# Optimization experiments

Measured on AMD Instinct MI355X. Metric: run time of the kernel, lower is better.

The kernel has to match this reference:

```python
import jax, jax.numpy as jnp
import numpy as np

# dims: B batch, N regions, F feature, L max seq len, A att size, E embed, D decode, V vocab
B, N, F, L, A, E, D, V = 256, 36, 2048, 26, 512, 1024, 1024, 10000
T = L - 1  # max decode steps
ARNET_W = 0.005


def _lstm(x, h, c, wih, whh, b):
    # torch.nn.LSTMCell math (b = b_ih + b_hh fused)
    g = x @ wih.T + h @ whh.T + b
    i, f, gg, o = jnp.split(g, 4, axis=1)
    c2 = jax.nn.sigmoid(f) * c + jax.nn.sigmoid(i) * jnp.tanh(gg)
    return jax.nn.sigmoid(o) * jnp.tanh(c2), c2


def setup_inputs():
    key = jax.random.key(0)
    ks = jax.random.split(key, 21)
    p = lambda k, s: jax.random.normal(k, s, jnp.float32) * 0.02
    feats = jax.random.normal(ks[0], (B, N, F), jnp.float32)
    sequences = jax.random.randint(ks[1], (B, L), 0, V)
    sizes = jax.random.randint(ks[2], (B, 1), 2, L + 1).at[0, 0].set(L)  # pin max length
    return dict(
        feats=feats, sequences=sequences, sizes=sizes,
        emb=p(ks[3], (V, E)),
        td_wih=p(ks[4], (4 * D, E + F + D)), td_whh=p(ks[5], (4 * D, D)), td_b=p(ks[6], (4 * D,)),
        lang_wih=p(ks[7], (4 * D, F + D)), lang_whh=p(ks[8], (4 * D, D)), lang_b=p(ks[9], (4 * D,)),
        attf_w=p(ks[10], (A, F)), attf_b=p(ks[11], (A,)),
        attd_w=p(ks[12], (A, D)), attd_b=p(ks[13], (A,)),
        att_w=p(ks[14], (A,)), att_b=p(ks[15], (1,)),
        out_w=p(ks[16], (V, D)), out_b=jnp.zeros((V,), jnp.float32),
        ar_wih=p(ks[17], (4 * D, D)), ar_whh=p(ks[18], (4 * D, D)), ar_b=p(ks[19], (4 * D,)),
        arl_w=p(ks[20], (D, D)), arl_b=jnp.zeros((D,), jnp.float32),
    )


def reference(feats, sequences, sizes, emb, td_wih, td_whh, td_b,
              lang_wih, lang_whh, lang_b, attf_w, attf_b, attd_w, attd_b,
              att_w, att_b, out_w, out_b, ar_wih, ar_whh, ar_b, arl_w, arl_b):
    # sort by length descending so the active set at each step is a batch prefix
    order = jnp.argsort(-sizes[:, 0])
    dec_len = sizes[order, 0] - 1          # [B]
    seq = sequences[order]                 # [B,L]
    fs = feats[order]                      # [B,N,F]
    favg = jnp.mean(fs, axis=1)            # [B,F]
    embs = emb[seq]                        # [B,L,E]
    # feature projection of the attention module is step-invariant -> hoist
    img_att = jnp.einsum('bnf,af->bna', fs, attf_w) + attf_b  # [B,N,A]

    dt = feats.dtype
    z = jnp.zeros((B, D), dt)
    carry0 = (z, z, z, z, z, z, z, jnp.zeros((), dt))

    def step(carry, xs):
        h1, c1, h2, c2, arh, arc, prev_h1, loss = carry
        e_t, t = xs
        act = t < dec_len                  # [B] rows still decoding
        am = act[:, None]
        bsz = jnp.sum(act.astype(dt))
        # top-down attention LSTM
        h1n, c1n = _lstm(jnp.concatenate([h2, favg, e_t], axis=1), h1, c1, td_wih, td_whh, td_b)
        # additive (Bahdanau) attention; dropout is identity in eval mode
        q = h1n @ attd_w.T + attd_b        # [B,A]
        scores = jnp.einsum('bna,a->bn', jax.nn.relu(q[:, None, :] + img_att), att_w) + att_b[0]
        alpha = jax.nn.softmax(scores, axis=1)
        aw = jnp.einsum('bn,bnf->bf', alpha, fs)
        # language LSTM
        h2n, c2n = _lstm(jnp.concatenate([aw, h1n], axis=1), h2, c2, lang_wih, lang_whh, lang_b)
        # arnet auxiliary LSTM reconstructing previous hidden1
        arhn, arcn = _lstm(h1n, arh, arc, ar_wih, ar_whh, ar_b)
        diff = arhn @ arl_w.T + arl_b - prev_h1
        step_loss = jnp.where(
            t > 0,
            jnp.sum(jnp.where(act, jnp.sum(diff * diff, axis=1), 0.0)) / jnp.maximum(bsz, 1.0) * ARNET_W,
            0.0)
        pred_t = jnp.where(am, h2n @ out_w.T + out_b, 0.0)  # inactive rows stay zero
        upd = lambda new, old: jnp.where(am, new, old)      # freeze state of finished rows
        carry = (upd(h1n, h1), upd(c1n, c1), upd(h2n, h2), upd(c2n, c2),
                 upd(arhn, arh), upd(arcn, arc), upd(h1n, prev_h1), loss + step_loss)
        return carry, pred_t

    xs = (jnp.swapaxes(embs[:, :T], 0, 1), jnp.arange(T))
    carry, preds = jax.lax.scan(step, carry0, xs)
    return jnp.swapaxes(preds, 0, 1), carry[-1]  # preds [B,T,V], loss_ar scalar
```

## Files before the change

### kernel.cpp

```cpp
#include <hip/hip_runtime.h>
#include <hip/hip_bf16.h>
#include <cstdio>

typedef __hip_bfloat16 bf16;
using s8v   = __attribute__((ext_vector_type(8))) short;
using f32x4 = __attribute__((ext_vector_type(4))) float;

#define BB    256
#define NIMG  36
#define FDIM  2048
#define LSEQ  26
#define TSTEP 25
#define ADIM  512
#define EDIM  1024
#define DDIM  1024
#define VDIM  10000
#define G4    4096
#define N3    4608
#define K1    5120
#define K2    4096
#define K3    2048
#define SPLT  8

__device__ inline float bf2f(bf16 x){ return __bfloat162float(x); }
__device__ inline bf16  f2bf(float x){ return __float2bfloat16(x); }
__device__ inline float sig_(float x){ return 1.0f/(1.0f + __expf(-x)); }
__device__ inline float tanh_(float x){ return tanhf(x); }

__device__ __forceinline__ void gl_lds16(const void* g, void* l){
  __builtin_amdgcn_global_load_lds(
      (__attribute__((address_space(1))) void*)g,
      (__attribute__((address_space(3))) void*)l, 16, 0, 0);
}

template<int BM, int BN>
__global__ __launch_bounds__(256, 2) void gemm_bt(
    const bf16* __restrict__ A, int lda,
    const bf16* __restrict__ Bw, int ldb,
    float* __restrict__ C, long ldc,
    int M, int Nreal, int Ktot, int nsplit,
    const float* __restrict__ bias,
    const int* __restrict__ rowmap,
    const int* __restrict__ mask,
    const int* __restrict__ nact, int t)
{
  constexpr int BK = 32;
  constexpr int AHALF = BM*BK;
  constexpr int HALF  = (BM+BN)*BK;
  __shared__ bf16 lds[2*HALF];

  const int bn = blockIdx.x, bm = blockIdx.y, bz = blockIdx.z;
  if (nact && (long)bm*BM >= (long)nact[t]) return;

  const int tid  = threadIdx.x;
  const int lane = tid & 63;
  const int wave = tid >> 6;
  const int wr = wave & 1, wc = wave >> 1;
  constexpr int TM = BM/32, TN = BN/32;

  const int ks   = Ktot / nsplit;
  const int kbeg = bz * ks;
  const long arow0 = (long)bm*BM;
  const long bcol0 = (long)bn*BN;

  constexpr int AIT = (BM*4)/256;
  constexpr int BIT = (BN*4)/256;
  const bf16* agp[AIT]; int alo[AIT];
  const bf16* bgp[BIT]; int blo[BIT];
#pragma unroll
  for (int u=0;u<AIT;u++){
    int c = tid + u*256; int r = c>>2, sl = c&3;
    int q = sl ^ ((r>>1)&3);
    long sr = arow0 + r;
    if (rowmap) sr = rowmap[sr];
    agp[u] = A + sr*(long)lda + kbeg + q*8;
    alo[u] = c*8;
  }
#pragma unroll
  for (int u=0;u<BIT;u++){
    int c = tid + u*256; int r = c>>2, sl = c&3;
    int q = sl ^ ((r>>1)&3);
    long gc = bcol0 + r;
    bgp[u] = Bw + ((gc < (long)Nreal) ? gc : 0)*(long)ldb + kbeg + q*8;
    blo[u] = AHALF + c*8;
  }

  f32x4 acc[TM][TN];
#pragma unroll
  for (int i=0;i<TM;i++)
#pragma unroll
    for (int j=0;j<TN;j++) acc[i][j] = (f32x4){0.f,0.f,0.f,0.f};

  const int m0 = lane & 15;
  const int co = (((lane>>4) ^ ((m0>>1)&3)) * 8);
  int aoff[TM], boff[TN];
#pragma unroll
  for (int i=0;i<TM;i++) aoff[i] = (wr*(BM/2) + i*16 + m0)*BK + co;
#pragma unroll
  for (int j=0;j<TN;j++) boff[j] = AHALF + (wc*(BN/2) + j*16 + m0)*BK + co;

#pragma unroll
  for (int u=0;u<AIT;u++) gl_lds16(agp[u], lds + alo[u]);
#pragma unroll
  for (int u=0;u<BIT;u++) gl_lds16(bgp[u], lds + blo[u]);
  __syncthreads();

  auto phase = [&](int bc, int bp, int kc){
    const int kp = kc + BK;
    if (kp < ks) {
      bf16* Pb = lds + bp*HALF;
#pragma unroll
      for (int u=0;u<AIT;u++) gl_lds16(agp[u] + kp, Pb + alo[u]);
#pragma unroll
      for (int u=0;u<BIT;u++) gl_lds16(bgp[u] + kp, Pb + blo[u]);
    }
    const bf16* Lb = lds + bc*HALF;
    s8v afr[TM], bfr[TN];
#pragma unroll
    for (int i=0;i<TM;i++) afr[i] = *(const s8v*)(Lb + aoff[i]);
#pragma unroll
    for (int j=0;j<TN;j++) bfr[j] = *(const s8v*)(Lb + boff[j]);
#pragma unroll
    for (int i=0;i<TM;i++)
#pragma unroll
      for (int j=0;j<TN;j++)
        acc[i][j] = __builtin_amdgcn_mfma_f32_16x16x32_bf16(afr[i], bfr[j], acc[i][j], 0, 0, 0);
    __syncthreads();
  };
  for (int kc = 0; kc < ks; kc += 2*BK) {
    phase(0, 1, kc);
    phase(1, 0, kc + BK);
  }

  float* Cz = C + (long)bz * (long)M * ldc;
  const int rq = lane >> 4;
#pragma unroll
  for (int i=0;i<TM;i++){
    long row = arow0 + wr*(BM/2) + i*16 + rq*4;
#pragma unroll
    for (int j=0;j<TN;j++){
      long col = bcol0 + wc*(BN/2) + j*16 + m0;
      if (col < (long)Nreal) {
        float bv = (bias != nullptr && bz == 0) ? bias[col] : 0.f;
#pragma unroll
        for (int r=0;r<4;r++){
          float v = acc[i][j][r] + bv;
          if (mask) v = (t < mask[row + r]) ? v : 0.f;
          Cz[(row + r)*ldc + col] = v;
        }
      }
    }
  }
}

__global__ __launch_bounds__(256) void sort_kernel(
    const int* __restrict__ sizesp, int* __restrict__ order,
    int* __restrict__ dec, float* __restrict__ bszf, int* __restrict__ nact,
    int* __restrict__ rowmap)
{
  __shared__ int ssz[BB], so[BB], sd[BB];
  int b = threadIdx.x;
  ssz[b] = sizesp[b];
  __syncthreads();
  int s = ssz[b];
  int rank = 0;
  for (int j=0;j<BB;j++){
    int sj = ssz[j];
    rank += (sj > s) || (sj == s && j < b);
  }
  so[rank] = b;
  sd[rank] = s - 1;
  __syncthreads();
  order[b] = so[b];
  dec[b]   = sd[b];
  if (b < TSTEP){
    int c=0;
    for (int j=0;j<BB;j++) c += (sd[j] > b);
    bszf[b] = (float)(c > 0 ? c : 1);
    nact[b] = c;
  }
  for (int r=b; r<BB*NIMG; r+=BB) rowmap[r] = so[r/NIMG]*NIMG + (r%NIMG);
}

__global__ __launch_bounds__(256) void zero_f32(float* __restrict__ pz, long n){
  long i = (long)blockIdx.x*256 + threadIdx.x;
  if (i < n) pz[i] = 0.f;
}

__global__ __launch_bounds__(256) void f2b_kernel(
    const float* __restrict__ s, bf16* __restrict__ d, long n)
{
  long i = ((long)blockIdx.x*256 + threadIdx.x)*8;
  if (i >= n) return;
  float4 a = *(const float4*)(s+i);
  float4 b = *(const float4*)(s+i+4);
  bf16 t[8] = {f2bf(a.x),f2bf(a.y),f2bf(a.z),f2bf(a.w),
               f2bf(b.x),f2bf(b.y),f2bf(b.z),f2bf(b.w)};
  *(uint4*)(d+i) = *(uint4*)t;
}

__global__ __launch_bounds__(256) void init_xcat(
    bf16* __restrict__ x1, bf16* __restrict__ x2, bf16* __restrict__ x3)
{
  int idx = blockIdx.x*256 + threadIdx.x;
  int b = idx >> 10, d = idx & 1023;
  bf16 z = f2bf(0.f);
  x1[(long)b*K1 + d]        = z;
  x1[(long)b*K1 + 4096 + d] = z;
  x2[(long)b*K2 + 3072 + d] = z;
  x3[(long)b*K3 + 1024 + d] = z;
}

__global__ __launch_bounds__(256) void favg_kernel(
    const float* __restrict__ feats, const int* __restrict__ order,
    bf16* __restrict__ x1)
{
  int idx = blockIdx.x*256 + threadIdx.x;
  int b = idx >> 11, f = idx & 2047;
  const float* fb = feats + (long)order[b]*NIMG*FDIM + f;
  float s = 0.f;
#pragma unroll 4
  for (int n=0;n<NIMG;n++) s += fb[n*FDIM];
  x1[(long)b*K1 + 1024 + f] = f2bf(s * (1.0f/36.0f));
}

__global__ __launch_bounds__(256) void concat2_f(
    bf16* __restrict__ dst, const float* __restrict__ s1, int k1,
    const float* __restrict__ s2, int k2, int rows)
{
  long nch = (long)rows*(k1+k2)/8;
  long c = (long)blockIdx.x*256 + threadIdx.x;
  if (c >= nch) return;
  long e = c*8;
  int ld = k1+k2;
  long r = e / ld; int col = (int)(e % ld);
  const float* src = (col < k1) ? (s1 + r*(long)k1 + col) : (s2 + r*(long)k2 + (col - k1));
  float4 a = *(const float4*)src;
  float4 b = *(const float4*)(src+4);
  bf16 t[8] = {f2bf(a.x),f2bf(a.y),f2bf(a.z),f2bf(a.w),
               f2bf(b.x),f2bf(b.y),f2bf(b.z),f2bf(b.w)};
  *(uint4*)(dst + e) = *(uint4*)t;
}

__global__ __launch_bounds__(256) void w3_attd_f(
    bf16* __restrict__ w3, const float* __restrict__ attd_w)
{
  long c = (long)blockIdx.x*256 + threadIdx.x;
  long e = c*8;
  long r = e / 2048; int col = (int)(e % 2048);
  bf16 t[8];
  if (col < 1024){
    const float* src = attd_w + r*1024 + col;
    float4 a = *(const float4*)src;
    float4 b = *(const float4*)(src+4);
    t[0]=f2bf(a.x); t[1]=f2bf(a.y); t[2]=f2bf(a.z); t[3]=f2bf(a.w);
    t[4]=f2bf(b.x); t[5]=f2bf(b.y); t[6]=f2bf(b.z); t[7]=f2bf(b.w);
  } else {
    bf16 z = f2bf(0.f);
#pragma unroll
    for (int u=0;u<8;u++) t[u]=z;
  }
  *(uint4*)(w3 + (4096 + r)*2048 + col) = *(uint4*)t;
}

__global__ __launch_bounds__(256) void attb_kernel(
    const float* __restrict__ a, const float* __restrict__ b, float* __restrict__ o)
{
  int i = blockIdx.x*256 + threadIdx.x;
  if (i < ADIM) o[i] = a[i] + b[i];
}

__global__ __launch_bounds__(256) void embed_kernel(
    const int* __restrict__ seqs, const int* __restrict__ order,
    const float* __restrict__ emb, int t, const int* __restrict__ nact,
    bf16* __restrict__ x1)
{
  int idx = blockIdx.x*256 + threadIdx.x;
  int b = idx >> 10, e = idx & 1023;
  if (b >= nact[t]) return;
  int tok = seqs[order[b]*LSEQ + t];
  x1[(long)b*K1 + 3072 + e] = f2bf(emb[(long)tok*EDIM + e]);
}

__global__ __launch_bounds__(256) void gates1_kernel(
    const float* __restrict__ g, const float* __restrict__ bias,
    const float* __restrict__ h_old, float* __restrict__ h_new,
    float* __restrict__ c, const int* __restrict__ nact, int t,
    bf16* __restrict__ x1, bf16* __restrict__ x2, bf16* __restrict__ x3)
{
  int idx = blockIdx.x*256 + threadIdx.x;
  int b = idx >> 10, d = idx & 1023;
  if (b >= nact[t]) { h_new[idx] = h_old[idx]; return; }
  float gi=0,gf=0,gg=0,go=0;
#pragma unroll
  for (int z=0; z<SPLT; z++){
    const float* gz = g + (long)z*BB*G4 + (long)b*G4;
    gi += gz[d]; gf += gz[d+1024]; gg += gz[d+2048]; go += gz[d+3072];
  }
  gi += bias[d]; gf += bias[d+1024]; gg += bias[d+2048]; go += bias[d+3072];
  float cn = sig_(gf)*c[idx] + sig_(gi)*tanh_(gg);
  float hn = sig_(go)*tanh_(cn);
  h_new[idx] = hn;
  c[idx] = cn;
  x1[(long)b*K1 + 4096 + d] = f2bf(hn);
  x2[(long)b*K2 + 2048 + d] = f2bf(hn);
  x3[(long)b*K3 + d]        = f2bf(hn);
}

__global__ __launch_bounds__(256) void gates2_kernel(
    const float* __restrict__ g, const float* __restrict__ bias,
    float* __restrict__ h2s, float* __restrict__ c2s,
    const int* __restrict__ nact, int t,
    bf16* __restrict__ h2n_bf, bf16* __restrict__ x1, bf16* __restrict__ x2)
{
  int idx = blockIdx.x*256 + threadIdx.x;
  int b = idx >> 10, d = idx & 1023;
  if (b >= nact[t]) return;
  float gi=0,gf=0,gg=0,go=0;
#pragma unroll
  for (int z=0; z<SPLT; z++){
    const float* gz = g + (long)z*BB*G4 + (long)b*G4;
    gi += gz[d]; gf += gz[d+1024]; gg += gz[d+2048]; go += gz[d+3072];
  }
  gi += bias[d]; gf += bias[d+1024]; gg += bias[d+2048]; go += bias[d+3072];
  float cn = sig_(gf)*c2s[idx] + sig_(gi)*tanh_(gg);
  float hn = sig_(go)*tanh_(cn);
  h2s[idx] = hn;
  c2s[idx] = cn;
  h2n_bf[idx] = f2bf(hn);
  x1[(long)b*K1 + d]        = f2bf(hn);
  x2[(long)b*K2 + 3072 + d] = f2bf(hn);
}

__global__ __launch_bounds__(256) void gates3_kernel(
    const float* __restrict__ g, const float* __restrict__ bias,
    float* __restrict__ arh, float* __restrict__ arc,
    const int* __restrict__ nact, int t,
    bf16* __restrict__ arhn_bf, bf16* __restrict__ x3)
{
  int idx = blockIdx.x*256 + threadIdx.x;
  int b = idx >> 10, d = idx & 1023;
  if (b >= nact[t]) return;
  float gi=0,gf=0,gg=0,go=0;
#pragma unroll
  for (int z=0; z<4; z++){
    const float* gz = g + (long)z*BB*N3 + (long)b*N3;
    gi += gz[d]; gf += gz[d+1024]; gg += gz[d+2048]; go += gz[d+3072];
  }
  gi += bias[d]; gf += bias[d+1024]; gg += bias[d+2048]; go += bias[d+3072];
  float cn = sig_(gf)*arc[idx] + sig_(gi)*tanh_(gg);
  float hn = sig_(go)*tanh_(cn);
  arh[idx] = hn;
  arc[idx] = cn;
  arhn_bf[idx] = f2bf(hn);
  x3[(long)b*K3 + 1024 + d] = f2bf(hn);
}

__global__ __launch_bounds__(256) void scores_kernel(
    const float* __restrict__ g3,
    const float* __restrict__ imgatt,
    const float* __restrict__ att_w, const float* __restrict__ att_b,
    const int* __restrict__ nact, int t,
    float* __restrict__ scores)
{
  int gw = blockIdx.x*4 + (threadIdx.x >> 6);
  if (gw >= BB*NIMG) return;
  int b = gw / NIMG;
  if (b >= nact[t]) return;
  int lane = threadIdx.x & 63;
  const float* q0 = g3 + (long)b*N3 + 4096;
  const float* ia = imgatt + (long)gw*ADIM;
  float s = 0.f;
#pragma unroll
  for (int u=0; u<8; u++){
    int a = u*64 + lane;
    float v = q0[a] + q0[(long)BB*N3 + a] + q0[2L*BB*N3 + a] + q0[3L*BB*N3 + a] + ia[a];
    v = fmaxf(v, 0.f);
    s += v * att_w[a];
  }
  for (int off=32; off; off>>=1) s += __shfl_down(s, off);
  if (lane == 0) scores[gw] = s + att_b[0];
}

__global__ __launch_bounds__(256) void attn_kernel(
    const float* __restrict__ scores, const bf16* __restrict__ feats_bf,
    const int* __restrict__ order, const int* __restrict__ nact, int t,
    bf16* __restrict__ x2)
{
  int b = blockIdx.x;
  if (b >= nact[t]) return;
  __shared__ float alpha[NIMG];
  int tid = threadIdx.x;
  if (tid < 64) {
    float v = (tid < NIMG) ? scores[b*NIMG + tid] : -1e30f;
    float m = v;
    for (int off=32; off; off>>=1) m = fmaxf(m, __shfl_down(m, off));
    m = __shfl(m, 0);
    float e = (tid < NIMG) ? __expf(v - m) : 0.f;
    float sum = e;
    for (int off=32; off; off>>=1) sum += __shfl_down(sum, off);
    sum = __shfl(sum, 0);
    if (tid < NIMG) alpha[tid] = e / sum;
  }
  __syncthreads();
  const bf16* fsb = feats_bf + (long)order[b]*NIMG*FDIM;
  int f0 = tid*8;
  float s[8] = {0.f,0.f,0.f,0.f,0.f,0.f,0.f,0.f};
#pragma unroll 4
  for (int n=0; n<NIMG; n++){
    float al = alpha[n];
    bf16 v[8]; *(s8v*)v = *(const s8v*)(fsb + (long)n*FDIM + f0);
#pragma unroll
    for (int u=0;u<8;u++) s[u] += al * bf2f(v[u]);
  }
  bf16 o[8];
#pragma unroll
  for (int u=0;u<8;u++) o[u] = f2bf(s[u]);
  *(uint4*)(x2 + (long)b*K2 + f0) = *(uint4*)o;
}

__global__ __launch_bounds__(256) void loss_kernel(
    const float* __restrict__ arl_out,
    const float* __restrict__ h_old,
    const int* __restrict__ nact, const float* __restrict__ bszf,
    int t, float* __restrict__ loss)
{
  if (t == 0) return;
  int b = blockIdx.x;
  if (b >= nact[t]) return;
  const long SDL = (long)BB*DDIM;
  float s = 0.f;
  for (int d = threadIdx.x; d < DDIM; d += 256) {
    long i = (long)b*DDIM + d;
    float v = arl_out[i] + arl_out[SDL + i] + arl_out[2*SDL + i] + arl_out[3*SDL + i]
            - h_old[i];
    s += v*v;
  }
  __shared__ float red[4];
  for (int off=32; off; off>>=1) s += __shfl_down(s, off);
  if ((threadIdx.x & 63) == 0) red[threadIdx.x >> 6] = s;
  __syncthreads();
  if (threadIdx.x == 0) {
    float tot = red[0]+red[1]+red[2]+red[3];
    atomicAdd(loss, tot * (0.005f / bszf[t]));
  }
}

__global__ void finalize_kernel(const float* __restrict__ loss, float* __restrict__ out){
  if (threadIdx.x == 0) out[(long)BB*TSTEP*VDIM] = *loss;
}

extern "C" void kernel_launch(void* const* d_in, const int* in_sizes, int n_in,
                              void* d_out, int out_size, void* d_ws, size_t ws_size,
                              hipStream_t stream) {
  const float* feats    = (const float*)d_in[0];
  const int*   seqs     = (const int*)d_in[1];
  const int*   sizesp   = (const int*)d_in[2];
  const float* emb      = (const float*)d_in[3];
  const float* td_wih   = (const float*)d_in[4];
  const float* td_whh   = (const float*)d_in[5];
  const float* td_b     = (const float*)d_in[6];
  const float* lang_wih = (const float*)d_in[7];
  const float* lang_whh = (const float*)d_in[8];
  const float* lang_b   = (const float*)d_in[9];
  const float* attf_w   = (const float*)d_in[10];
  const float* attf_b   = (const float*)d_in[11];
  const float* attd_w   = (const float*)d_in[12];
  const float* attd_b   = (const float*)d_in[13];
  const float* att_w    = (const float*)d_in[14];
  const float* att_b    = (const float*)d_in[15];
  const float* out_w    = (const float*)d_in[16];
  const float* out_b    = (const float*)d_in[17];
  const float* ar_wih   = (const float*)d_in[18];
  const float* ar_whh   = (const float*)d_in[19];
  const float* ar_b     = (const float*)d_in[20];
  const float* arl_w    = (const float*)d_in[21];
  const float* arl_b    = (const float*)d_in[22];
  float* out = (float*)d_out;

  char* p = (char*)d_ws;
  auto alloc = [&](size_t n) -> void* {
    void* r = (void*)p; p += ((n + 255) & ~(size_t)255); return r;
  };
  const long SD = (long)BB*DDIM;

  int*   order    = (int*)  alloc(BB*4);
  int*   dec      = (int*)  alloc(BB*4);
  float* bszf     = (float*)alloc(TSTEP*4);
  int*   nact     = (int*)  alloc(TSTEP*4);
  int*   rowmap   = (int*)  alloc(BB*NIMG*4);
  float* stateblk = (float*)alloc((7*SD + 64)*4);
  bf16*  W1       = (bf16*) alloc((size_t)G4*K1*2);
  bf16*  W2       = (bf16*) alloc((size_t)G4*K2*2);
  bf16*  W3       = (bf16*) alloc((size_t)N3*K3*2);
  bf16*  feats_bf = (bf16*) alloc((size_t)BB*NIMG*FDIM*2);
  bf16*  attf_bf  = (bf16*) alloc((size_t)ADIM*FDIM*2);
  bf16*  outw_bf  = (bf16*) alloc((size_t)VDIM*DDIM*2);
  bf16*  arlw_bf  = (bf16*) alloc((size_t)DDIM*DDIM*2);
  bf16*  xcat1    = (bf16*) alloc((size_t)BB*K1*2);
  bf16*  xcat2    = (bf16*) alloc((size_t)BB*K2*2);
  bf16*  xcat3    = (bf16*) alloc((size_t)BB*K3*2);
  bf16*  h2n_bf   = (bf16*) alloc((size_t)BB*DDIM*2);
  bf16*  arhn_bf  = (bf16*) alloc((size_t)BB*DDIM*2);
  float* g12      = (float*)alloc((size_t)SPLT*BB*G4*4);
  float* arl_out  = (float*)alloc((size_t)4*BB*DDIM*4);
  float* imgatt   = (float*)alloc((size_t)BB*NIMG*ADIM*4);
  float* scorebuf = (float*)alloc((size_t)BB*NIMG*4);
  float* attb     = (float*)alloc((size_t)ADIM*4);
  float* g3       = g12;

  size_t need = (size_t)(p - (char*)d_ws);
  if (need > ws_size) {
    fprintf(stderr, "kernel_launch: ws too small: need %zu have %zu\n", need, ws_size);
    return;
  }

  float* h1A = stateblk;
  float* h1B = stateblk + SD;
  float* c1  = stateblk + 2*SD;
  float* h2s = stateblk + 3*SD;
  float* c2s = stateblk + 4*SD;
  float* arh = stateblk + 5*SD;
  float* arc = stateblk + 6*SD;
  float* loss = stateblk + 7*SD;

  sort_kernel<<<1, 256, 0, stream>>>(sizesp, order, dec, bszf, nact, rowmap);
  long nz = 7*SD + 64;
  zero_f32<<<(int)((nz + 255)/256), 256, 0, stream>>>(stateblk, nz);
  long nout = (long)BB*TSTEP*VDIM;
  zero_f32<<<(int)((nout + 255)/256), 256, 0, stream>>>(out, nout);
  init_xcat<<<1024, 256, 0, stream>>>(xcat1, xcat2, xcat3);
  favg_kernel<<<2048, 256, 0, stream>>>(feats, order, xcat1);
  f2b_kernel<<<9216, 256, 0, stream>>>(feats,  feats_bf, (long)BB*NIMG*FDIM);
  f2b_kernel<<< 512, 256, 0, stream>>>(attf_w, attf_bf,  (long)ADIM*FDIM);
  f2b_kernel<<<5000, 256, 0, stream>>>(out_w,  outw_bf,  (long)VDIM*DDIM);
  f2b_kernel<<< 512, 256, 0, stream>>>(arl_w,  arlw_bf,  (long)DDIM*DDIM);
  concat2_f<<<10240, 256, 0, stream>>>(W1, td_wih, 4096, td_whh, 1024, 4096);
  concat2_f<<< 8192, 256, 0, stream>>>(W2, lang_wih, 3072, lang_whh, 1024, 4096);
  concat2_f<<< 4096, 256, 0, stream>>>(W3, ar_wih, 1024, ar_whh, 1024, 4096);
  w3_attd_f<<<512, 256, 0, stream>>>(W3, attd_w);
  attb_kernel<<<2, 256, 0, stream>>>(attf_b, attd_b, attb);
  gemm_bt<128,128><<<dim3(4,72,1), 256, 0, stream>>>(
      feats_bf, FDIM, attf_bf, FDIM, imgatt, (long)ADIM, BB*NIMG, ADIM, FDIM, 1,
      attb, rowmap, nullptr, nullptr, 0);

  for (int t = 0; t < TSTEP; t++) {
    float* h1old = (t & 1) ? h1B : h1A;
    float* h1new = (t & 1) ? h1A : h1B;

    embed_kernel<<<1024, 256, 0, stream>>>(seqs, order, emb, t, nact, xcat1);

    gemm_bt<128,128><<<dim3(32,2,SPLT), 256, 0, stream>>>(
        xcat1, K1, W1, K1, g12, (long)G4, BB, G4, K1, SPLT,
        nullptr, nullptr, nullptr, nact, t);
    gates1_kernel<<<1024, 256, 0, stream>>>(
        g12, td_b, h1old, h1new, c1, nact, t, xcat1, xcat2, xcat3);

    gemm_bt<128,128><<<dim3(36,2,4), 256, 0, stream>>>(
        xcat3, K3, W3, K3, g3, (long)N3, BB, N3, K3, 4,
        nullptr, nullptr, nullptr, nact, t);
    gates3_kernel<<<1024, 256, 0, stream>>>(
        g3, ar_b, arh, arc, nact, t, arhn_bf, xcat3);

    scores_kernel<<<2304, 256, 0, stream>>>(
        g3, imgatt, att_w, att_b, nact, t, scorebuf);
    attn_kernel<<<256, 256, 0, stream>>>(scorebuf, feats_bf, order, nact, t, xcat2);

    gemm_bt<128,128><<<dim3(32,2,SPLT), 256, 0, stream>>>(
        xcat2, K2, W2, K2, g12, (long)G4, BB, G4, K2, SPLT,
        nullptr, nullptr, nullptr, nact, t);
    gates2_kernel<<<1024, 256, 0, stream>>>(
        g12, lang_b, h2s, c2s, nact, t, h2n_bf, xcat1, xcat2);

    gemm_bt<64,64><<<dim3(16,4,4), 256, 0, stream>>>(
        arhn_bf, DDIM, arlw_bf, DDIM, arl_out, (long)DDIM, BB, DDIM, DDIM, 4,
        arl_b, nullptr, nullptr, nact, t);
    loss_kernel<<<256, 256, 0, stream>>>(arl_out, h1old, nact, bszf, t, loss);

    gemm_bt<128,64><<<dim3(157,2,1), 256, 0, stream>>>(
        h2n_bf, DDIM, outw_bf, DDIM, out + (long)t*VDIM, (long)TSTEP*VDIM,
        BB, VDIM, DDIM, 1, out_b, nullptr, dec, nact, t);
  }

  finalize_kernel<<<1, 64, 0, stream>>>(loss, out);
}
```

Baseline: 3.566 ms.

## Fuse per-step GEMMs into dual launches, triple-buffer LDS, merge elementwise kernels

Replaces the GEMM with a 1D-grid dual-problem kernel so independent GEMMs share one launch: the language LSTM with the arnet projection, and the vocab projection with the next step's top-down GEMM. The GEMM main loop moves from double to triple buffering with explicit vmcnt waits. gates3+scores+attention and gates2+embedding+loss become single kernels, and the split-K factors drop (8 to 4, 4 to 2). Launch count and partial-sum traffic go down, at the cost of more LDS per block and fewer blocks for the split-K GEMMs.

Result: faster. 2.942 ms (-17.5%).

```diff
diff --git a/kernel.cpp b/kernel.cpp
--- a/kernel.cpp
+++ b/kernel.cpp
@@ -20,7 +20,8 @@
 #define K1    5120
 #define K2    4096
 #define K3    2048
-#define SPLT  8
+#define SPLT  4
+#define SPLTA 2
 
 __device__ inline float bf2f(bf16 x){ return __bfloat162float(x); }
 __device__ inline bf16  f2bf(float x){ return __float2bfloat16(x); }
@@ -33,24 +34,30 @@
       (__attribute__((address_space(3))) void*)l, 16, 0, 0);
 }
 
+struct GArgs {
+  const bf16* A; const bf16* Bw; float* C;
+  const float* bias; const int* rowmap; const int* mask;
+  long ldc;
+  int lda, ldb, M, Nreal, Ktot, nsplit, nbx, nby, tt, use_nact;
+};
+
 template<int BM, int BN>
-__global__ __launch_bounds__(256, 2) void gemm_bt(
-    const bf16* __restrict__ A, int lda,
-    const bf16* __restrict__ Bw, int ldb,
-    float* __restrict__ C, long ldc,
-    int M, int Nreal, int Ktot, int nsplit,
-    const float* __restrict__ bias,
-    const int* __restrict__ rowmap,
-    const int* __restrict__ mask,
-    const int* __restrict__ nact, int t)
+__global__ __launch_bounds__(256, 2) void gemm_dual(
+    GArgs a0, GArgs a1, int nblk0, const int* __restrict__ nact)
 {
   constexpr int BK = 32;
   constexpr int AHALF = BM*BK;
   constexpr int HALF  = (BM+BN)*BK;
-  __shared__ bf16 lds[2*HALF];
-
-  const int bn = blockIdx.x, bm = blockIdx.y, bz = blockIdx.z;
-  if (nact && (long)bm*BM >= (long)nact[t]) return;
+  __shared__ bf16 lds[3*HALF];
+
+  int id = blockIdx.x;
+  GArgs g = (id < nblk0) ? a0 : a1;
+  if (id >= nblk0) id -= nblk0;
+  const int bz  = id / (g.nbx * g.nby);
+  const int rem = id - bz*(g.nbx*g.nby);
+  const int bm  = rem / g.nbx;
+  const int bn  = rem - bm*g.nbx;
+  if (g.use_nact && (long)bm*BM >= (long)nact[g.tt]) return;
 
   const int tid  = threadIdx.x;
   const int lane = tid & 63;
@@ -58,7 +65,7 @@
   const int wr = wave & 1, wc = wave >> 1;
   constexpr int TM = BM/32, TN = BN/32;
 
-  const int ks   = Ktot / nsplit;
+  const int ks   = g.Ktot / g.nsplit;
   const int kbeg = bz * ks;
   const long arow0 = (long)bm*BM;
   const long bcol0 = (long)bn*BN;
@@ -72,8 +79,8 @@
     int c = tid + u*256; int r = c>>2, sl = c&3;
     int q = sl ^ ((r>>1)&3);
     long sr = arow0 + r;
-    if (rowmap) sr = rowmap[sr];
-    agp[u] = A + sr*(long)lda + kbeg + q*8;
+    if (g.rowmap) sr = g.rowmap[sr];
+    agp[u] = g.A + sr*(long)g.lda + kbeg + q*8;
     alo[u] = c*8;
   }
 #pragma unroll
@@ -81,7 +88,7 @@
     int c = tid + u*256; int r = c>>2, sl = c&3;
     int q = sl ^ ((r>>1)&3);
     long gc = bcol0 + r;
-    bgp[u] = Bw + ((gc < (long)Nreal) ? gc : 0)*(long)ldb + kbeg + q*8;
+    bgp[u] = g.Bw + ((gc < (long)g.Nreal) ? gc : 0)*(long)g.ldb + kbeg + q*8;
     blo[u] = AHALF + c*8;
   }
 
@@ -99,22 +106,14 @@
 #pragma unroll
   for (int j=0;j<TN;j++) boff[j] = AHALF + (wc*(BN/2) + j*16 + m0)*BK + co;
 
-#pragma unroll
-  for (int u=0;u<AIT;u++) gl_lds16(agp[u], lds + alo[u]);
-#pragma unroll
-  for (int u=0;u<BIT;u++) gl_lds16(bgp[u], lds + blo[u]);
-  __syncthreads();
-
-  auto phase = [&](int bc, int bp, int kc){
-    const int kp = kc + BK;
-    if (kp < ks) {
-      bf16* Pb = lds + bp*HALF;
-#pragma unroll
-      for (int u=0;u<AIT;u++) gl_lds16(agp[u] + kp, Pb + alo[u]);
-#pragma unroll
-      for (int u=0;u<BIT;u++) gl_lds16(bgp[u] + kp, Pb + blo[u]);
-    }
-    const bf16* Lb = lds + bc*HALF;
+  auto stage = [&](int koff, int lbase){
+#pragma unroll
+    for (int u=0;u<AIT;u++) gl_lds16(agp[u] + koff, lds + lbase + alo[u]);
+#pragma unroll
+    for (int u=0;u<BIT;u++) gl_lds16(bgp[u] + koff, lds + lbase + blo[u]);
+  };
+  auto compute = [&](int lbase){
+    const bf16* Lb = lds + lbase;
     s8v afr[TM], bfr[TN];
 #pragma unroll
     for (int i=0;i<TM;i++) afr[i] = *(const s8v*)(Lb + aoff[i]);
@@ -125,14 +124,31 @@
 #pragma unroll
       for (int j=0;j<TN;j++)
         acc[i][j] = __builtin_amdgcn_mfma_f32_16x16x32_bf16(afr[i], bfr[j], acc[i][j], 0, 0, 0);
-    __syncthreads();
   };
-  for (int kc = 0; kc < ks; kc += 2*BK) {
-    phase(0, 1, kc);
-    phase(1, 0, kc + BK);
-  }
-
-  float* Cz = C + (long)bz * (long)M * ldc;
+
+  const int nt = ks / BK;
+  stage(0, 0);
+  stage(BK, HALF);
+  int bc = 0;
+  for (int k = 0; k < nt-1; ++k){
+    __builtin_amdgcn_sched_barrier(0);
+    asm volatile("s_waitcnt vmcnt(%0)" :: "n"(AIT+BIT) : "memory");
+    __builtin_amdgcn_s_barrier();
+    __builtin_amdgcn_sched_barrier(0);
+    if (k+2 < nt){
+      int bp = bc+2; if (bp >= 3) bp -= 3;
+      stage((k+2)*BK, bp*HALF);
+    }
+    compute(bc*HALF);
+    bc = (bc+1 == 3) ? 0 : bc+1;
+  }
+  __builtin_amdgcn_sched_barrier(0);
+  asm volatile("s_waitcnt vmcnt(0)" ::: "memory");
+  __builtin_amdgcn_s_barrier();
+  __builtin_amdgcn_sched_barrier(0);
+  compute(bc*HALF);
+
+  float* Cz = g.C + (long)bz * (long)g.M * g.ldc;
   const int rq = lane >> 4;
 #pragma unroll
   for (int i=0;i<TM;i++){
@@ -140,13 +156,13 @@
 #pragma unroll
     for (int j=0;j<TN;j++){
       long col = bcol0 + wc*(BN/2) + j*16 + m0;
-      if (col < (long)Nreal) {
-        float bv = (bias != nullptr && bz == 0) ? bias[col] : 0.f;
+      if (col < (long)g.Nreal) {
+        float bv = (g.bias != nullptr && bz == 0) ? g.bias[col] : 0.f;
 #pragma unroll
         for (int r=0;r<4;r++){
           float v = acc[i][j][r] + bv;
-          if (mask) v = (t < mask[row + r]) ? v : 0.f;
-          Cz[(row + r)*ldc + col] = v;
+          if (g.mask) v = (g.tt < g.mask[row + r]) ? v : 0.f;
+          Cz[(row + r)*g.ldc + col] = v;
         }
       }
     }
@@ -272,12 +288,10 @@
 
 __global__ __launch_bounds__(256) void embed_kernel(
     const int* __restrict__ seqs, const int* __restrict__ order,
-    const float* __restrict__ emb, int t, const int* __restrict__ nact,
-    bf16* __restrict__ x1)
+    const float* __restrict__ emb, int t, bf16* __restrict__ x1)
 {
   int idx = blockIdx.x*256 + threadIdx.x;
   int b = idx >> 10, e = idx & 1023;
-  if (b >= nact[t]) return;
   int tok = seqs[order[b]*LSEQ + t];
   x1[(long)b*K1 + 3072 + e] = f2bf(emb[(long)tok*EDIM + e]);
 }
@@ -307,92 +321,65 @@
   x3[(long)b*K3 + d]        = f2bf(hn);
 }
 
-__global__ __launch_bounds__(256) void gates2_kernel(
-    const float* __restrict__ g, const float* __restrict__ bias,
-    float* __restrict__ h2s, float* __restrict__ c2s,
-    const int* __restrict__ nact, int t,
-    bf16* __restrict__ h2n_bf, bf16* __restrict__ x1, bf16* __restrict__ x2)
-{
-  int idx = blockIdx.x*256 + threadIdx.x;
-  int b = idx >> 10, d = idx & 1023;
-  if (b >= nact[t]) return;
-  float gi=0,gf=0,gg=0,go=0;
-#pragma unroll
-  for (int z=0; z<SPLT; z++){
-    const float* gz = g + (long)z*BB*G4 + (long)b*G4;
-    gi += gz[d]; gf += gz[d+1024]; gg += gz[d+2048]; go += gz[d+3072];
-  }
-  gi += bias[d]; gf += bias[d+1024]; gg += bias[d+2048]; go += bias[d+3072];
-  float cn = sig_(gf)*c2s[idx] + sig_(gi)*tanh_(gg);
-  float hn = sig_(go)*tanh_(cn);
-  h2s[idx] = hn;
-  c2s[idx] = cn;
-  h2n_bf[idx] = f2bf(hn);
-  x1[(long)b*K1 + d]        = f2bf(hn);
-  x2[(long)b*K2 + 3072 + d] = f2bf(hn);
-}
-
-__global__ __launch_bounds__(256) void gates3_kernel(
-    const float* __restrict__ g, const float* __restrict__ bias,
+__global__ __launch_bounds__(256) void gates3_attn_kernel(
+    const float* __restrict__ g,
+    const float* __restrict__ bias,
     float* __restrict__ arh, float* __restrict__ arc,
-    const int* __restrict__ nact, int t,
-    bf16* __restrict__ arhn_bf, bf16* __restrict__ x3)
-{
-  int idx = blockIdx.x*256 + threadIdx.x;
-  int b = idx >> 10, d = idx & 1023;
-  if (b >= nact[t]) return;
-  float gi=0,gf=0,gg=0,go=0;
-#pragma unroll
-  for (int z=0; z<4; z++){
-    const float* gz = g + (long)z*BB*N3 + (long)b*N3;
-    gi += gz[d]; gf += gz[d+1024]; gg += gz[d+2048]; go += gz[d+3072];
-  }
-  gi += bias[d]; gf += bias[d+1024]; gg += bias[d+2048]; go += bias[d+3072];
-  float cn = sig_(gf)*arc[idx] + sig_(gi)*tanh_(gg);
-  float hn = sig_(go)*tanh_(cn);
-  arh[idx] = hn;
-  arc[idx] = cn;
-  arhn_bf[idx] = f2bf(hn);
-  x3[(long)b*K3 + 1024 + d] = f2bf(hn);
-}
-
-__global__ __launch_bounds__(256) void scores_kernel(
-    const float* __restrict__ g3,
     const float* __restrict__ imgatt,
     const float* __restrict__ att_w, const float* __restrict__ att_b,
+    const bf16* __restrict__ feats_bf, const int* __restrict__ order,
     const int* __restrict__ nact, int t,
-    float* __restrict__ scores)
-{
-  int gw = blockIdx.x*4 + (threadIdx.x >> 6);
-  if (gw >= BB*NIMG) return;
-  int b = gw / NIMG;
+    bf16* __restrict__ arhn_bf, bf16* __restrict__ x3, bf16* __restrict__ x2)
+{
+  int bid = blockIdx.x;
+  if (bid < 1024) {
+    int idx = bid*256 + threadIdx.x;
+    int b = idx >> 10, d = idx & 1023;
+    if (b >= nact[t]) return;
+    float gi=0,gf=0,gg=0,go=0;
+#pragma unroll
+    for (int z=0; z<4; z++){
+      const float* gz = g + (long)z*BB*N3 + (long)b*N3;
+      gi += gz[d]; gf += gz[d+1024]; gg += gz[d+2048]; go += gz[d+3072];
+    }
+    gi += bias[d]; gf += bias[d+1024]; gg += bias[d+2048]; go += bias[d+3072];
+    float cn = sig_(gf)*arc[idx] + sig_(gi)*tanh_(gg);
+    float hn = sig_(go)*tanh_(cn);
+    arh[idx] = hn;
+    arc[idx] = cn;
+    arhn_bf[idx] = f2bf(hn);
+    x3[(long)b*K3 + 1024 + d] = f2bf(hn);
+    return;
+  }
+  int b = bid - 1024;
   if (b >= nact[t]) return;
-  int lane = threadIdx.x & 63;
-  const float* q0 = g3 + (long)b*N3 + 4096;
-  const float* ia = imgatt + (long)gw*ADIM;
-  float s = 0.f;
-#pragma unroll
-  for (int u=0; u<8; u++){
-    int a = u*64 + lane;
-    float v = q0[a] + q0[(long)BB*N3 + a] + q0[2L*BB*N3 + a] + q0[3L*BB*N3 + a] + ia[a];
-    v = fmaxf(v, 0.f);
-    s += v * att_w[a];
-  }
-  for (int off=32; off; off>>=1) s += __shfl_down(s, off);
-  if (lane == 0) scores[gw] = s + att_b[0];
-}
-
-__global__ __launch_bounds__(256) void attn_kernel(
-    const float* __restrict__ scores, const bf16* __restrict__ feats_bf,
-    const int* __restrict__ order, const int* __restrict__ nact, int t,
-    bf16* __restrict__ x2)
-{
-  int b = blockIdx.x;
-  if (b >= nact[t]) return;
+  __shared__ float qv[ADIM];
+  __shared__ float sc[NIMG];
   __shared__ float alpha[NIMG];
   int tid = threadIdx.x;
+  {
+    const float* q0 = g + (long)b*N3 + 4096;
+    for (int a = tid; a < ADIM; a += 256)
+      qv[a] = q0[a] + q0[(long)BB*N3 + a] + q0[2L*BB*N3 + a] + q0[3L*BB*N3 + a];
+  }
+  __syncthreads();
+  int wv = tid >> 6, ln = tid & 63;
+  for (int n = wv; n < NIMG; n += 4){
+    const float* ia = imgatt + ((long)b*NIMG + n)*ADIM;
+    float s = 0.f;
+#pragma unroll
+    for (int u=0; u<8; u++){
+      int a = u*64 + ln;
+      float v = qv[a] + ia[a];
+      v = fmaxf(v, 0.f);
+      s += v * att_w[a];
+    }
+    for (int off=32; off; off>>=1) s += __shfl_down(s, off);
+    if (ln == 0) sc[n] = s + att_b[0];
+  }
+  __syncthreads();
   if (tid < 64) {
-    float v = (tid < NIMG) ? scores[b*NIMG + tid] : -1e30f;
+    float v = (tid < NIMG) ? sc[tid] : -1e30f;
     float m = v;
     for (int off=32; off; off>>=1) m = fmaxf(m, __shfl_down(m, off));
     m = __shfl(m, 0);
@@ -419,21 +406,49 @@
   *(uint4*)(x2 + (long)b*K2 + f0) = *(uint4*)o;
 }
 
-__global__ __launch_bounds__(256) void loss_kernel(
-    const float* __restrict__ arl_out,
-    const float* __restrict__ h_old,
-    const int* __restrict__ nact, const float* __restrict__ bszf,
-    int t, float* __restrict__ loss)
-{
+__global__ __launch_bounds__(256) void gates2_emb_loss_kernel(
+    const float* __restrict__ g, const float* __restrict__ bias,
+    float* __restrict__ h2s, float* __restrict__ c2s,
+    const int* __restrict__ nact, int t,
+    bf16* __restrict__ h2n_bf, bf16* __restrict__ x1, bf16* __restrict__ x2,
+    const int* __restrict__ seqs, const int* __restrict__ order,
+    const float* __restrict__ emb,
+    const float* __restrict__ arl_out, const float* __restrict__ h_old,
+    const float* __restrict__ bszf, float* __restrict__ loss)
+{
+  int bid = blockIdx.x;
+  if (bid < 1024) {
+    int idx = bid*256 + threadIdx.x;
+    int b = idx >> 10, d = idx & 1023;
+    if (t+1 < TSTEP && b < nact[t+1]) {
+      int tok = seqs[order[b]*LSEQ + (t+1)];
+      x1[(long)b*K1 + 3072 + d] = f2bf(emb[(long)tok*EDIM + d]);
+    }
+    if (b >= nact[t]) return;
+    float gi=0,gf=0,gg=0,go=0;
+#pragma unroll
+    for (int z=0; z<SPLT; z++){
+      const float* gz = g + (long)z*BB*G4 + (long)b*G4;
+      gi += gz[d]; gf += gz[d+1024]; gg += gz[d+2048]; go += gz[d+3072];
+    }
+    gi += bias[d]; gf += bias[d+1024]; gg += bias[d+2048]; go += bias[d+3072];
+    float cn = sig_(gf)*c2s[idx] + sig_(gi)*tanh_(gg);
+    float hn = sig_(go)*tanh_(cn);
+    h2s[idx] = hn;
+    c2s[idx] = cn;
+    h2n_bf[idx] = f2bf(hn);
+    x1[(long)b*K1 + d]        = f2bf(hn);
+    x2[(long)b*K2 + 3072 + d] = f2bf(hn);
+    return;
+  }
   if (t == 0) return;
-  int b = blockIdx.x;
+  int b = bid - 1024;
   if (b >= nact[t]) return;
   const long SDL = (long)BB*DDIM;
   float s = 0.f;
   for (int d = threadIdx.x; d < DDIM; d += 256) {
     long i = (long)b*DDIM + d;
-    float v = arl_out[i] + arl_out[SDL + i] + arl_out[2*SDL + i] + arl_out[3*SDL + i]
-            - h_old[i];
+    float v = arl_out[i] + arl_out[SDL + i] - h_old[i];
     s += v*v;
   }
   __shared__ float red[4];
@@ -502,12 +517,10 @@
   bf16*  xcat3    = (bf16*) alloc((size_t)BB*K3*2);
   bf16*  h2n_bf   = (bf16*) alloc((size_t)BB*DDIM*2);
   bf16*  arhn_bf  = (bf16*) alloc((size_t)BB*DDIM*2);
-  float* g12      = (float*)alloc((size_t)SPLT*BB*G4*4);
-  float* arl_out  = (float*)alloc((size_t)4*BB*DDIM*4);
+  float* g12      = (float*)alloc((size_t)4*BB*N3*4);
+  float* arl_out  = (float*)alloc((size_t)SPLTA*BB*DDIM*4);
   float* imgatt   = (float*)alloc((size_t)BB*NIMG*ADIM*4);
-  float* scorebuf = (float*)alloc((size_t)BB*NIMG*4);
   float* attb     = (float*)alloc((size_t)ADIM*4);
-  float* g3       = g12;
 
   size_t need = (size_t)(p - (char*)d_ws);
   if (need > ws_size) {
@@ -523,6 +536,14 @@
   float* arh = stateblk + 5*SD;
   float* arc = stateblk + 6*SD;
   float* loss = stateblk + 7*SD;
+
+  auto mkargs = [](const bf16* A,int lda,const bf16* Bw,int ldb,float* C,long ldc,
+                   int M,int Nreal,int Ktot,int ns,const float* bias,
+                   const int* rowmap,const int* mask,int nbx,int nby,int tt,int un){
+    GArgs g; g.A=A; g.Bw=Bw; g.C=C; g.bias=bias; g.rowmap=rowmap; g.mask=mask;
+    g.ldc=ldc; g.lda=lda; g.ldb=ldb; g.M=M; g.Nreal=Nreal; g.Ktot=Ktot; g.nsplit=ns;
+    g.nbx=nbx; g.nby=nby; g.tt=tt; g.use_nact=un; return g;
+  };
 
   sort_kernel<<<1, 256, 0, stream>>>(sizesp, order, dec, bszf, nact, rowmap);
   long nz = 7*SD + 64;
@@ -540,46 +561,51 @@
   concat2_f<<< 4096, 256, 0, stream>>>(W3, ar_wih, 1024, ar_whh, 1024, 4096);
   w3_attd_f<<<512, 256, 0, stream>>>(W3, attd_w);
   attb_kernel<<<2, 256, 0, stream>>>(attf_b, attd_b, attb);
-  gemm_bt<128,128><<<dim3(4,72,1), 256, 0, stream>>>(
-      feats_bf, FDIM, attf_bf, FDIM, imgatt, (long)ADIM, BB*NIMG, ADIM, FDIM, 1,
-      attb, rowmap, nullptr, nullptr, 0);
+
+  GArgs ia = mkargs(feats_bf, FDIM, attf_bf, FDIM, imgatt, ADIM,
+                    BB*NIMG, ADIM, FDIM, 1, attb, rowmap, nullptr, 4, 72, 0, 0);
+  gemm_dual<128,128><<<288, 256, 0, stream>>>(ia, ia, 288, nact);
+
+  embed_kernel<<<1024, 256, 0, stream>>>(seqs, order, emb, 0, xcat1);
+  GArgs td0 = mkargs(xcat1, K1, W1, K1, g12, G4, BB, G4, K1, SPLT,
+                     nullptr, nullptr, nullptr, 32, 2, 0, 1);
+  gemm_dual<128,128><<<32*2*SPLT, 256, 0, stream>>>(td0, td0, 32*2*SPLT, nact);
 
   for (int t = 0; t < TSTEP; t++) {
     float* h1old = (t & 1) ? h1B : h1A;
     float* h1new = (t & 1) ? h1A : h1B;
 
-    embed_kernel<<<1024, 256, 0, stream>>>(seqs, order, emb, t, nact, xcat1);
-
-    gemm_bt<128,128><<<dim3(32,2,SPLT), 256, 0, stream>>>(
-        xcat1, K1, W1, K1, g12, (long)G4, BB, G4, K1, SPLT,
-        nullptr, nullptr, nullptr, nact, t);
     gates1_kernel<<<1024, 256, 0, stream>>>(
         g12, td_b, h1old, h1new, c1, nact, t, xcat1, xcat2, xcat3);
 
-    gemm_bt<128,128><<<dim3(36,2,4), 256, 0, stream>>>(
-        xcat3, K3, W3, K3, g3, (long)N3, BB, N3, K3, 4,
-        nullptr, nullptr, nullptr, nact, t);
-    gates3_kernel<<<1024, 256, 0, stream>>>(
-        g3, ar_b, arh, arc, nact, t, arhn_bf, xcat3);
-
-    scores_kernel<<<2304, 256, 0, stream>>>(
-        g3, imgatt, att_w, att_b, nact, t, scorebuf);
-    attn_kernel<<<256, 256, 0, stream>>>(scorebuf, feats_bf, order, nact, t, xcat2);
-
-    gemm_bt<128,128><<<dim3(32,2,SPLT), 256, 0, stream>>>(
-        xcat2, K2, W2, K2, g12, (long)G4, BB, G4, K2, SPLT,
-        nullptr, nullptr, nullptr, nact, t);
-    gates2_kernel<<<1024, 256, 0, stream>>>(
-        g12, lang_b, h2s, c2s, nact, t, h2n_bf, xcat1, xcat2);
-
-    gemm_bt<64,64><<<dim3(16,4,4), 256, 0, stream>>>(
-        arhn_bf, DDIM, arlw_bf, DDIM, arl_out, (long)DDIM, BB, DDIM, DDIM, 4,
-        arl_b, nullptr, nullptr, nact, t);
-    loss_kernel<<<256, 256, 0, stream>>>(arl_out, h1old, nact, bszf, t, loss);
-
-    gemm_bt<128,64><<<dim3(157,2,1), 256, 0, stream>>>(
-        h2n_bf, DDIM, outw_bf, DDIM, out + (long)t*VDIM, (long)TSTEP*VDIM,
-        BB, VDIM, DDIM, 1, out_b, nullptr, dec, nact, t);
+    GArgs ar = mkargs(xcat3, K3, W3, K3, g12, N3, BB, N3, K3, 4,
+                      nullptr, nullptr, nullptr, 36, 2, t, 1);
+    gemm_dual<128,128><<<36*2*4, 256, 0, stream>>>(ar, ar, 36*2*4, nact);
+
+    gates3_attn_kernel<<<1280, 256, 0, stream>>>(
+        g12, ar_b, arh, arc, imgatt, att_w, att_b, feats_bf, order,
+        nact, t, arhn_bf, xcat3, xcat2);
+
+    GArgs lg = mkargs(xcat2, K2, W2, K2, g12, G4, BB, G4, K2, SPLT,
+                      nullptr, nullptr, nullptr, 32, 2, t, 1);
+    GArgs al = mkargs(arhn_bf, DDIM, arlw_bf, DDIM, arl_out, DDIM,
+                      BB, DDIM, DDIM, SPLTA, arl_b, nullptr, nullptr, 8, 2, t, 1);
+    gemm_dual<128,128><<<32*2*SPLT + 8*2*SPLTA, 256, 0, stream>>>(lg, al, 32*2*SPLT, nact);
+
+    gates2_emb_loss_kernel<<<1280, 256, 0, stream>>>(
+        g12, lang_b, h2s, c2s, nact, t, h2n_bf, xcat1, xcat2,
+        seqs, order, emb, arl_out, h1old, bszf, loss);
+
+    GArgs vo = mkargs(h2n_bf, DDIM, outw_bf, DDIM, out + (long)t*VDIM,
+                      (long)TSTEP*VDIM, BB, VDIM, DDIM, 1,
+                      out_b, nullptr, dec, 79, 2, t, 1);
+    if (t + 1 < TSTEP) {
+      GArgs tn = mkargs(xcat1, K1, W1, K1, g12, G4, BB, G4, K1, SPLT,
+                        nullptr, nullptr, nullptr, 32, 2, t+1, 1);
+      gemm_dual<128,128><<<79*2 + 32*2*SPLT, 256, 0, stream>>>(vo, tn, 79*2, nact);
+    } else {
+      gemm_dual<128,128><<<79*2, 256, 0, stream>>>(vo, vo, 79*2, nact);
+    }
   }
 
   finalize_kernel<<<1, 64, 0, stream>>>(loss, out);
```
